# Kernel optimization log

Measured on AMD Instinct MI355X. Metric: run time of the kernel, lower is better.

The kernel has to match this reference:

```python
import jax, jax.numpy as jnp
import numpy as np

HEAD_NUM = 7
HEAD_DIM = 64
HIDDEN = 896

def rotate_half(t):
    d = t.shape[-1] // 2
    return jnp.concatenate([-t[..., d:], t[..., :d]], axis=-1)

def setup_inputs() -> dict:
    key = jax.random.key(0)
    ks = jax.random.split(key, 11)
    B, S = 4, 2048
    proj = HEAD_NUM * HEAD_DIM  # 448
    sc_in = 1.0 / np.sqrt(HIDDEN)
    sc_pr = 1.0 / np.sqrt(proj)
    pos = jnp.arange(S)[:, None].astype(jnp.float32)
    inv_freq = 1.0 / (10000.0 ** (jnp.arange(0, HEAD_DIM, 2, dtype=jnp.float32) / HEAD_DIM))
    ang = pos * inv_freq[None, :]              # [S, D/2]
    emb = jnp.concatenate([ang, ang], axis=-1) # [S, D]
    return {
        'x': jax.random.normal(ks[0], (B, S, HIDDEN), jnp.float32),
        'cos': jnp.cos(emb),
        'sin': jnp.sin(emb),
        'q_w': jax.random.normal(ks[1], (proj, HIDDEN), jnp.float32) * sc_in,
        'q_b': jax.random.normal(ks[2], (proj,), jnp.float32) * 0.01,
        'k_w': jax.random.normal(ks[3], (proj, HIDDEN), jnp.float32) * sc_in,
        'k_b': jax.random.normal(ks[4], (proj,), jnp.float32) * 0.01,
        'v_w': jax.random.normal(ks[5], (proj, HIDDEN), jnp.float32) * sc_in,
        'v_b': jax.random.normal(ks[6], (proj,), jnp.float32) * 0.01,
        'o_w': jax.random.normal(ks[7], (HIDDEN, proj), jnp.float32) * sc_pr,
        'o_b': jax.random.normal(ks[8], (HIDDEN,), jnp.float32) * 0.01,
    }

def reference(x, cos, sin, q_w, q_b, k_w, k_b, v_w, v_b, o_w, o_b):
    B, S, _ = x.shape
    def proj(w, b):
        y = jnp.einsum('bsh,ph->bsp', x, w) + b          # [B,S,H*D]
        return y.reshape(B, S, HEAD_NUM, HEAD_DIM).transpose(0, 2, 1, 3)  # [B,H,S,D]
    q = proj(q_w, q_b)
    k = proj(k_w, k_b)
    v = proj(v_w, v_b)
    c = cos[None, None, :, :]
    s = sin[None, None, :, :]
    q = q * c + rotate_half(q) * s
    k = k * c + rotate_half(k) * s
    scores = jnp.einsum('bhqd,bhkd->bhqk', q, k) / np.sqrt(HEAD_DIM)
    attn = jax.nn.softmax(scores, axis=-1)
    out = jnp.einsum('bhqk,bhkd->bhqd', attn, v)          # [B,H,S,D]
    out = out.transpose(0, 2, 1, 3).reshape(B, S, HEAD_NUM * HEAD_DIM)
    return jnp.einsum('bsp,hp->bsh', out, o_w) + o_b
```

## Files before the change

kernel.cpp:

```cpp
#include <hip/hip_runtime.h>

typedef _Float16 f16;
typedef __attribute__((ext_vector_type(8))) _Float16 f16x8;
typedef __attribute__((ext_vector_type(4))) _Float16 f16x4;
typedef __attribute__((ext_vector_type(4))) float f32x4;

#define MFMA(a,b,c) __builtin_amdgcn_mfma_f32_16x16x32_f16(a,b,c,0,0,0)

constexpr int HN = 7, HD = 64, HID = 896, PR = 448;
constexpr int NB = 4, NS = 2048, NM = NB * NS;
constexpr float LOG2E = 1.44269504088896f;

__device__ __forceinline__ void gload16(const f16* g, f16* l) {
    __builtin_amdgcn_global_load_lds(
        (const __attribute__((address_space(1))) void*)g,
        (__attribute__((address_space(3))) void*)l,
        16, 0, 0);
}

__global__ __launch_bounds__(256) void conv_kernel(
    const float* __restrict__ x,  const float* __restrict__ qw,
    const float* __restrict__ kw, const float* __restrict__ vw,
    const float* __restrict__ ow,
    f16* __restrict__ xb, f16* __restrict__ wq, f16* __restrict__ wk,
    f16* __restrict__ wv, f16* __restrict__ wo)
{
    const int XV = NM * HID / 4;
    const int WV = PR * HID / 4;
    const int TOT = XV + 4 * WV;
    int64_t stride = (int64_t)gridDim.x * blockDim.x;
    for (int64_t v = (int64_t)blockIdx.x * 256 + threadIdx.x; v < TOT; v += stride) {
        const float* src; f16* dst; int64_t off;
        if (v < XV)               { src = x;  dst = xb; off = v; }
        else if (v < XV + WV)     { src = qw; dst = wq; off = v - XV; }
        else if (v < XV + 2*WV)   { src = kw; dst = wk; off = v - XV - WV; }
        else if (v < XV + 3*WV)   { src = vw; dst = wv; off = v - XV - 2*WV; }
        else                      { src = ow; dst = wo; off = v - XV - 3*WV; }
        f32x4 fv = *((const f32x4*)src + off);
        f16x4 hv = { (f16)fv[0], (f16)fv[1], (f16)fv[2], (f16)fv[3] };
        *((f16x4*)dst + off) = hv;
    }
}

__global__ __launch_bounds__(256) void qkv_gemm(
    const f16* __restrict__ xb, const f16* __restrict__ wq,
    const f16* __restrict__ wk, const f16* __restrict__ wv,
    const float* __restrict__ qb, const float* __restrict__ kb,
    const float* __restrict__ vb,
    const float* __restrict__ cosT, const float* __restrict__ sinT,
    f16* __restrict__ Q, f16* __restrict__ K, f16* __restrict__ Vt)
{
    extern __shared__ char smem[];
    f16*  As = (f16*)smem;
    f16*  Bs = (f16*)(smem + 128*64*2);
    float* Cs = (float*)smem;

    const int ty = blockIdx.x / 7;
    const int nt = blockIdx.x % 7;
    const int mt = blockIdx.y;
    const int m0 = mt * 128, n0 = nt * 64;

    const f16* w = (ty == 0) ? wq : (ty == 1) ? wk : wv;
    const float* bias = (ty == 0) ? qb : (ty == 1) ? kb : vb;

    const int tid = threadIdx.x;
    const int wid = tid >> 6, lane = tid & 63;
    const int wm = wid >> 1, wn = wid & 1;
    const int lg = lane >> 4, lr = lane & 15;

    f32x4 acc[4][2] = {};

    for (int k0 = 0; k0 < HID; k0 += 64) {
        #pragma unroll
        for (int p = 0; p < 4; p++) {
            int r = p*32 + (tid >> 3), c = tid & 7;
            f16x8 v = *(const f16x8*)(xb + (int64_t)(m0 + r)*HID + k0 + c*8);
            *(f16x8*)(As + r*64 + ((c ^ (r & 7)) * 8)) = v;
        }
        #pragma unroll
        for (int p = 0; p < 2; p++) {
            int r = p*32 + (tid >> 3), c = tid & 7;
            f16x8 v = *(const f16x8*)(w + (int64_t)(n0 + r)*HID + k0 + c*8);
            *(f16x8*)(Bs + r*64 + ((c ^ (r & 7)) * 8)) = v;
        }
        __syncthreads();
        #pragma unroll
        for (int kc = 0; kc < 2; kc++) {
            f16x8 af[4], bf[2];
            #pragma unroll
            for (int fm = 0; fm < 4; fm++) {
                int r = wm*64 + fm*16 + lr;
                int c = kc*4 + lg;
                af[fm] = *(const f16x8*)(As + r*64 + ((c ^ (r & 7)) * 8));
            }
            #pragma unroll
            for (int fn = 0; fn < 2; fn++) {
                int r = wn*32 + fn*16 + lr;
                int c = kc*4 + lg;
                bf[fn] = *(const f16x8*)(Bs + r*64 + ((c ^ (r & 7)) * 8));
            }
            #pragma unroll
            for (int fm = 0; fm < 4; fm++)
                #pragma unroll
                for (int fn = 0; fn < 2; fn++)
                    acc[fm][fn] = MFMA(af[fm], bf[fn], acc[fm][fn]);
        }
        __syncthreads();
    }

    #pragma unroll
    for (int fm = 0; fm < 4; fm++)
        #pragma unroll
        for (int fn = 0; fn < 2; fn++)
            #pragma unroll
            for (int j = 0; j < 4; j++) {
                int r = wm*64 + fm*16 + lg*4 + j;
                int c = wn*32 + fn*16 + lr;
                Cs[r*65 + c] = acc[fm][fn][j] + bias[n0 + c];
            }
    __syncthreads();

    const int b = m0 / NS;
    const int s0 = m0 % NS;
    const int64_t bhbase = ((int64_t)(b*HN + nt)) * NS * HD;
    if (ty < 2) {
        const float scale = (ty == 0) ? 0.125f * LOG2E : 1.0f;
        int r = tid >> 1, d0 = (tid & 1) * 32;
        int s = s0 + r;
        f16 vals[32];
        #pragma unroll
        for (int i = 0; i < 32; i++) {
            int d = d0 + i;
            float y  = Cs[r*65 + d];
            float yo = Cs[r*65 + (d ^ 32)];
            float rot = (d < 32) ? -yo : yo;
            float val = (y * cosT[s*64 + d] + rot * sinT[s*64 + d]) * scale;
            vals[i] = (f16)val;
        }
        if (ty == 0) {
            f16* p = Q + bhbase + (int64_t)s * HD + d0;
            #pragma unroll
            for (int i = 0; i < 4; i++)
                *(f16x8*)(p + i*8) = *(f16x8*)(vals + i*8);
        } else {
            int tt = (s0 >> 6) + (r >> 6);
            int rt = r & 63;
            f16* base = K + bhbase + tt*4096 + rt*64;
            #pragma unroll
            for (int i = 0; i < 4; i++) {
                int pos = ((d0 >> 3) + i) ^ (rt & 7);
                *(f16x8*)(base + pos*8) = *(f16x8*)(vals + i*8);
            }
        }
    } else {
        int d = tid >> 2, si = (tid & 3) * 32;
        f16 vals[32];
        #pragma unroll
        for (int i = 0; i < 32; i++)
            vals[i] = (f16)Cs[(si + i)*65 + d];
        int tt = (s0 >> 6) + (si >> 6);
        int sb = si & 63;
        f16* base = Vt + bhbase + tt*4096 + d*64;
        #pragma unroll
        for (int i = 0; i < 4; i++) {
            int pos = ((sb >> 3) + i) ^ (d & 7);
            *(f16x8*)(base + pos*8) = *(f16x8*)(vals + i*8);
        }
    }
}

__global__ __launch_bounds__(256) void attn_kernel(
    const f16* __restrict__ Q, const f16* __restrict__ K2,
    const f16* __restrict__ V2, f16* __restrict__ O)
{
    __shared__ __align__(16) f16 KVs[2][2][4096];
    __shared__ __align__(16) f16 Pl[4][16][72];

    const int qb = blockIdx.x, bh = blockIdx.y;
    const int tid = threadIdx.x, w = tid >> 6, lane = tid & 63;
    const int g = lane >> 4, lr = lane & 15;
    const int q0 = qb * 64 + w * 16;

    const int64_t bhoff = (int64_t)bh * NS * HD;
    const f16* Qp = Q + bhoff;
    const f16* Kp = K2 + bhoff;
    const f16* Vp = V2 + bhoff;

    f16x8 aq0 = *(const f16x8*)(Qp + (q0 + lr) * HD + g * 8);
    f16x8 aq1 = *(const f16x8*)(Qp + (q0 + lr) * HD + 32 + g * 8);

    const int stoff = w * 1024 + lane * 8;
    const int ldoff = w * 1024;

    gload16(Kp + stoff,       &KVs[0][0][ldoff]);
    gload16(Kp + stoff + 512, &KVs[0][0][ldoff + 512]);
    gload16(Vp + stoff,       &KVs[0][1][ldoff]);
    gload16(Vp + stoff + 512, &KVs[0][1][ldoff + 512]);
    __syncthreads();

    f32x4 accO[4] = {};
    float mrun = -1e30f, srun = 0.f;

    const int ch0 = (g ^ (lr & 7)) * 8;
    const int ch1 = ((4 + g) ^ (lr & 7)) * 8;

    int buf = 0;
    for (int t = 0; t < NS / 64; ++t) {
        if (t + 1 < NS / 64) {
            const f16* ks = Kp + (t + 1) * 4096 + stoff;
            const f16* vs = Vp + (t + 1) * 4096 + stoff;
            gload16(ks,       &KVs[buf ^ 1][0][ldoff]);
            gload16(ks + 512, &KVs[buf ^ 1][0][ldoff + 512]);
            gload16(vs,       &KVs[buf ^ 1][1][ldoff]);
            gload16(vs + 512, &KVs[buf ^ 1][1][ldoff + 512]);
        }
        const f16* Ks = &KVs[buf][0][0];
        const f16* Vs = &KVs[buf][1][0];

        f32x4 sf[4];
        #pragma unroll
        for (int kt = 0; kt < 4; ++kt) {
            const f16* kl = Ks + (kt * 16 + lr) * 64;
            f16x8 k0 = *(const f16x8*)(kl + ch0);
            f16x8 k1 = *(const f16x8*)(kl + ch1);
            f32x4 z = {};
            z = MFMA(k0, aq0, z);
            z = MFMA(k1, aq1, z);
            sf[kt] = z;
        }

        float m00 = fmaxf(fmaxf(sf[0][0], sf[0][1]), fmaxf(sf[0][2], sf[0][3]));
        float m01 = fmaxf(fmaxf(sf[1][0], sf[1][1]), fmaxf(sf[1][2], sf[1][3]));
        float m10 = fmaxf(fmaxf(sf[2][0], sf[2][1]), fmaxf(sf[2][2], sf[2][3]));
        float m11 = fmaxf(fmaxf(sf[3][0], sf[3][1]), fmaxf(sf[3][2], sf[3][3]));
        float pmax = fmaxf(fmaxf(m00, m01), fmaxf(m10, m11));
        pmax = fmaxf(pmax, __shfl_xor(pmax, 16, 64));
        pmax = fmaxf(pmax, __shfl_xor(pmax, 32, 64));

        float mn = fmaxf(mrun, pmax);
        float corr = exp2f(mrun - mn);
        mrun = mn;

        float pf[16];
        #pragma unroll
        for (int kt = 0; kt < 4; ++kt)
            #pragma unroll
            for (int j = 0; j < 4; ++j)
                pf[kt*4 + j] = exp2f(sf[kt][j] - mn);

        float s0a = (pf[0] + pf[1]) + (pf[2] + pf[3]);
        float s1a = (pf[4] + pf[5]) + (pf[6] + pf[7]);
        float s2a = (pf[8] + pf[9]) + (pf[10] + pf[11]);
        float s3a = (pf[12] + pf[13]) + (pf[14] + pf[15]);
        float tsum = (s0a + s1a) + (s2a + s3a);
        tsum += __shfl_xor(tsum, 16, 64);
        tsum += __shfl_xor(tsum, 32, 64);
        srun = srun * corr + tsum;

        #pragma unroll
        for (int fn = 0; fn < 4; ++fn)
            #pragma unroll
            for (int j = 0; j < 4; ++j)
                accO[fn][j] *= corr;

        #pragma unroll
        for (int kt = 0; kt < 4; ++kt) {
            f16x4 pk = { (f16)pf[kt*4+0], (f16)pf[kt*4+1], (f16)pf[kt*4+2], (f16)pf[kt*4+3] };
            *(f16x4*)&Pl[w][lr][kt*16 + g*4] = pk;
        }
        f16x8 p0 = *(const f16x8*)&Pl[w][lr][g * 8];
        f16x8 p1 = *(const f16x8*)&Pl[w][lr][32 + g * 8];

        #pragma unroll
        for (int fn = 0; fn < 4; ++fn) {
            const f16* vl = Vs + (fn * 16 + lr) * 64;
            f16x8 v0 = *(const f16x8*)(vl + ch0);
            f16x8 v1 = *(const f16x8*)(vl + ch1);
            accO[fn] = MFMA(v0, p0, accO[fn]);
            accO[fn] = MFMA(v1, p1, accO[fn]);
        }
        __syncthreads();
        buf ^= 1;
    }

    const int b = bh / HN, h = bh % HN;
    const float inv = 1.0f / srun;
    const int q = q0 + lr;
    f16* orow = O + ((int64_t)b * NS + q) * PR + h * HD;
    #pragma unroll
    for (int fn = 0; fn < 4; ++fn) {
        f16x4 hv = { (f16)(accO[fn][0] * inv), (f16)(accO[fn][1] * inv),
                     (f16)(accO[fn][2] * inv), (f16)(accO[fn][3] * inv) };
        *(f16x4*)(orow + fn * 16 + g * 4) = hv;
    }
}

__global__ __launch_bounds__(256) void oproj_gemm(
    const f16* __restrict__ Ob, const f16* __restrict__ wo,
    const float* __restrict__ ob, float* __restrict__ out)
{
    extern __shared__ char smem[];
    f16* As = (f16*)smem;
    f16* Bs = (f16*)(smem + 128*64*2);

    const int nt = blockIdx.x, mt = blockIdx.y;
    const int m0 = mt*128, n0 = nt*64;
    const int tid = threadIdx.x;
    const int wid = tid >> 6, lane = tid & 63;
    const int wm = wid >> 1, wn = wid & 1;
    const int lg = lane >> 4, lr = lane & 15;

    f32x4 acc[4][2] = {};

    for (int k0 = 0; k0 < PR; k0 += 64) {
        #pragma unroll
        for (int p = 0; p < 4; p++) {
            int r = p*32 + (tid >> 3), c = tid & 7;
            f16x8 v = *(const f16x8*)(Ob + (int64_t)(m0 + r)*PR + k0 + c*8);
            *(f16x8*)(As + r*64 + ((c ^ (r & 7)) * 8)) = v;
        }
        #pragma unroll
        for (int p = 0; p < 2; p++) {
            int r = p*32 + (tid >> 3), c = tid & 7;
            f16x8 v = *(const f16x8*)(wo + (int64_t)(n0 + r)*PR + k0 + c*8);
            *(f16x8*)(Bs + r*64 + ((c ^ (r & 7)) * 8)) = v;
        }
        __syncthreads();
        #pragma unroll
        for (int kc = 0; kc < 2; kc++) {
            f16x8 af[4], bf[2];
            #pragma unroll
            for (int fm = 0; fm < 4; fm++) {
                int r = wm*64 + fm*16 + lr;
                int c = kc*4 + lg;
                af[fm] = *(const f16x8*)(As + r*64 + ((c ^ (r & 7)) * 8));
            }
            #pragma unroll
            for (int fn = 0; fn < 2; fn++) {
                int r = wn*32 + fn*16 + lr;
                int c = kc*4 + lg;
                bf[fn] = *(const f16x8*)(Bs + r*64 + ((c ^ (r & 7)) * 8));
            }
            #pragma unroll
            for (int fm = 0; fm < 4; fm++)
                #pragma unroll
                for (int fn = 0; fn < 2; fn++)
                    acc[fm][fn] = MFMA(af[fm], bf[fn], acc[fm][fn]);
        }
        __syncthreads();
    }

    #pragma unroll
    for (int fm = 0; fm < 4; fm++)
        #pragma unroll
        for (int fn = 0; fn < 2; fn++)
            #pragma unroll
            for (int j = 0; j < 4; j++) {
                int row = m0 + wm*64 + fm*16 + lg*4 + j;
                int col = n0 + wn*32 + fn*16 + lr;
                out[(int64_t)row*HID + col] = acc[fm][fn][j] + ob[col];
            }
}

extern "C" void kernel_launch(void* const* d_in, const int* in_sizes, int n_in,
                              void* d_out, int out_size, void* d_ws, size_t ws_size,
                              hipStream_t stream) {
    const float* x    = (const float*)d_in[0];
    const float* cosT = (const float*)d_in[1];
    const float* sinT = (const float*)d_in[2];
    const float* qw   = (const float*)d_in[3];
    const float* qb   = (const float*)d_in[4];
    const float* kw   = (const float*)d_in[5];
    const float* kb   = (const float*)d_in[6];
    const float* vw   = (const float*)d_in[7];
    const float* vb   = (const float*)d_in[8];
    const float* ow   = (const float*)d_in[9];
    const float* ob   = (const float*)d_in[10];
    float* out = (float*)d_out;

    char* ws = (char*)d_ws;
    f16* xb = (f16*)ws;  ws += (size_t)NM * HID * 2;
    f16* wqf = (f16*)ws; ws += (size_t)PR * HID * 2;
    f16* wkf = (f16*)ws; ws += (size_t)PR * HID * 2;
    f16* wvf = (f16*)ws; ws += (size_t)PR * HID * 2;
    f16* wof = (f16*)ws; ws += (size_t)HID * PR * 2;
    f16* Qb = (f16*)ws;  ws += (size_t)NB * HN * NS * HD * 2;
    f16* Kb = (f16*)ws;  ws += (size_t)NB * HN * NS * HD * 2;
    f16* Vt = (f16*)ws;  ws += (size_t)NB * HN * HD * NS * 2;
    f16* Obuf = (f16*)ws; ws += (size_t)NM * PR * 2;

    conv_kernel<<<dim3(2048), dim3(256), 0, stream>>>(x, qw, kw, vw, ow, xb, wqf, wkf, wvf, wof);
    qkv_gemm<<<dim3(21, 64), dim3(256), 33280, stream>>>(xb, wqf, wkf, wvf, qb, kb, vb, cosT, sinT, Qb, Kb, Vt);
    attn_kernel<<<dim3(32, 28), dim3(256), 0, stream>>>(Qb, Kb, Vt, Obuf);
    oproj_gemm<<<dim3(14, 64), dim3(256), 24576, stream>>>(Obuf, wof, ob, out);
}
```

Baseline: 256.6 us.

## Enlarge GEMM tiles, use direct LDS loads, XCD swizzle, lazy softmax rescale

The QKV and output-projection GEMMs get larger tiles (256x64 and 128x128) with 4x4 MFMA fragments per wave, and load global memory straight into LDS. The QKV epilogue now stages results in fp16 and handles full rows with vectorized cos/sin reads. All three main kernels remap block indices so neighbouring tiles land on the same XCD, which should improve L2 reuse. The attention kernel raises wave priority around its MFMA sections and skips the running-max rescale unless the max grows by more than a threshold. Staging in fp16 and the lazy rescale trade some numerical headroom for less work, and the larger tiles cut the number of blocks, which can leave CUs underused.

Result: no change. 254.5 us (-0.8%).

```diff
diff --git a/kernel.cpp b/kernel.cpp
--- a/kernel.cpp
+++ b/kernel.cpp
@@ -16,6 +16,10 @@
         (const __attribute__((address_space(1))) void*)g,
         (__attribute__((address_space(3))) void*)l,
         16, 0, 0);
+}
+
+__device__ __forceinline__ int xcd_swz(int orig, int per) {
+    return (orig & 7) * per + (orig >> 3);
 }
 
 __global__ __launch_bounds__(256) void conv_kernel(
@@ -51,121 +55,125 @@
     f16* __restrict__ Q, f16* __restrict__ K, f16* __restrict__ Vt)
 {
     extern __shared__ char smem[];
-    f16*  As = (f16*)smem;
-    f16*  Bs = (f16*)(smem + 128*64*2);
-    float* Cs = (float*)smem;
-
-    const int ty = blockIdx.x / 7;
-    const int nt = blockIdx.x % 7;
-    const int mt = blockIdx.y;
-    const int m0 = mt * 128, n0 = nt * 64;
+    f16* As = (f16*)smem;
+    f16* Bs = (f16*)(smem + 256*64*2);
+    f16* Cs = (f16*)smem;
+
+    const int wg = xcd_swz(blockIdx.x, 84);
+    const int tynt = wg % 21, mt = wg / 21;
+    const int ty = tynt / 7, nt = tynt % 7;
+    const int m0 = mt * 256, n0 = nt * 64;
 
     const f16* w = (ty == 0) ? wq : (ty == 1) ? wk : wv;
     const float* bias = (ty == 0) ? qb : (ty == 1) ? kb : vb;
 
     const int tid = threadIdx.x;
-    const int wid = tid >> 6, lane = tid & 63;
-    const int wm = wid >> 1, wn = wid & 1;
-    const int lg = lane >> 4, lr = lane & 15;
-
-    f32x4 acc[4][2] = {};
+    const int wv_ = tid >> 6, lane = tid & 63;
+    const int g = lane >> 4, lr = lane & 15;
+    const int lrow = lane >> 3;
+    const int cswz = (lane & 7) ^ (lrow & 7);
+
+    const int ch0 = ((0*4 + g) ^ (lr & 7)) * 8;
+    const int ch1 = ((1*4 + g) ^ (lr & 7)) * 8;
+
+    f32x4 acc[4][4] = {};
 
     for (int k0 = 0; k0 < HID; k0 += 64) {
         #pragma unroll
-        for (int p = 0; p < 4; p++) {
-            int r = p*32 + (tid >> 3), c = tid & 7;
-            f16x8 v = *(const f16x8*)(xb + (int64_t)(m0 + r)*HID + k0 + c*8);
-            *(f16x8*)(As + r*64 + ((c ^ (r & 7)) * 8)) = v;
+        for (int p = 0; p < 8; p++) {
+            int rt = wv_*64 + p*8;
+            gload16(xb + (int64_t)(m0 + rt + lrow)*HID + k0 + cswz*8, As + rt*64);
         }
         #pragma unroll
         for (int p = 0; p < 2; p++) {
-            int r = p*32 + (tid >> 3), c = tid & 7;
-            f16x8 v = *(const f16x8*)(w + (int64_t)(n0 + r)*HID + k0 + c*8);
-            *(f16x8*)(Bs + r*64 + ((c ^ (r & 7)) * 8)) = v;
+            int rt = wv_*16 + p*8;
+            gload16(w + (int64_t)(n0 + rt + lrow)*HID + k0 + cswz*8, Bs + rt*64);
         }
         __syncthreads();
         #pragma unroll
         for (int kc = 0; kc < 2; kc++) {
-            f16x8 af[4], bf[2];
-            #pragma unroll
-            for (int fm = 0; fm < 4; fm++) {
-                int r = wm*64 + fm*16 + lr;
-                int c = kc*4 + lg;
-                af[fm] = *(const f16x8*)(As + r*64 + ((c ^ (r & 7)) * 8));
-            }
-            #pragma unroll
-            for (int fn = 0; fn < 2; fn++) {
-                int r = wn*32 + fn*16 + lr;
-                int c = kc*4 + lg;
-                bf[fn] = *(const f16x8*)(Bs + r*64 + ((c ^ (r & 7)) * 8));
-            }
+            const int ch = kc ? ch1 : ch0;
+            f16x8 af[4], bf[4];
+            #pragma unroll
+            for (int fm = 0; fm < 4; fm++)
+                af[fm] = *(const f16x8*)(As + (wv_*64 + fm*16 + lr)*64 + ch);
+            #pragma unroll
+            for (int fn = 0; fn < 4; fn++)
+                bf[fn] = *(const f16x8*)(Bs + (fn*16 + lr)*64 + ch);
             #pragma unroll
             for (int fm = 0; fm < 4; fm++)
                 #pragma unroll
-                for (int fn = 0; fn < 2; fn++)
+                for (int fn = 0; fn < 4; fn++)
                     acc[fm][fn] = MFMA(af[fm], bf[fn], acc[fm][fn]);
         }
         __syncthreads();
     }
 
+    float bias_f[4];
+    #pragma unroll
+    for (int fn = 0; fn < 4; fn++) bias_f[fn] = bias[n0 + fn*16 + lr];
     #pragma unroll
     for (int fm = 0; fm < 4; fm++)
         #pragma unroll
-        for (int fn = 0; fn < 2; fn++)
-            #pragma unroll
-            for (int j = 0; j < 4; j++) {
-                int r = wm*64 + fm*16 + lg*4 + j;
-                int c = wn*32 + fn*16 + lr;
-                Cs[r*65 + c] = acc[fm][fn][j] + bias[n0 + c];
-            }
+        for (int fn = 0; fn < 4; fn++)
+            #pragma unroll
+            for (int j = 0; j < 4; j++)
+                Cs[(wv_*64 + fm*16 + g*4 + j)*72 + fn*16 + lr] = (f16)(acc[fm][fn][j] + bias_f[fn]);
     __syncthreads();
 
     const int b = m0 / NS;
     const int s0 = m0 % NS;
     const int64_t bhbase = ((int64_t)(b*HN + nt)) * NS * HD;
+
     if (ty < 2) {
         const float scale = (ty == 0) ? 0.125f * LOG2E : 1.0f;
-        int r = tid >> 1, d0 = (tid & 1) * 32;
-        int s = s0 + r;
-        f16 vals[32];
-        #pragma unroll
-        for (int i = 0; i < 32; i++) {
-            int d = d0 + i;
-            float y  = Cs[r*65 + d];
-            float yo = Cs[r*65 + (d ^ 32)];
-            float rot = (d < 32) ? -yo : yo;
-            float val = (y * cosT[s*64 + d] + rot * sinT[s*64 + d]) * scale;
-            vals[i] = (f16)val;
+        const int r = tid, s = s0 + r;
+        const f16* crow = Cs + r*72;
+        const float* cr = cosT + s*64;
+        const float* sr = sinT + s*64;
+        f16 vals[64];
+        #pragma unroll
+        for (int i = 0; i < 4; i++) {
+            f16x8 ylo = *(const f16x8*)(crow + i*8);
+            f16x8 yhi = *(const f16x8*)(crow + 32 + i*8);
+            #pragma unroll
+            for (int h = 0; h < 2; h++) {
+                f32x4 cl = *(const f32x4*)(cr + i*8 + h*4);
+                f32x4 sl = *(const f32x4*)(sr + i*8 + h*4);
+                f32x4 chh = *(const f32x4*)(cr + 32 + i*8 + h*4);
+                f32x4 shh = *(const f32x4*)(sr + 32 + i*8 + h*4);
+                #pragma unroll
+                for (int j = 0; j < 4; j++) {
+                    float lo = (float)ylo[h*4+j], hi = (float)yhi[h*4+j];
+                    vals[i*8 + h*4 + j]      = (f16)((lo*cl[j] - hi*sl[j]) * scale);
+                    vals[32 + i*8 + h*4 + j] = (f16)((hi*chh[j] + lo*shh[j]) * scale);
+                }
+            }
         }
         if (ty == 0) {
-            f16* p = Q + bhbase + (int64_t)s * HD + d0;
-            #pragma unroll
-            for (int i = 0; i < 4; i++)
+            f16* p = Q + bhbase + (int64_t)s * HD;
+            #pragma unroll
+            for (int i = 0; i < 8; i++)
                 *(f16x8*)(p + i*8) = *(f16x8*)(vals + i*8);
         } else {
             int tt = (s0 >> 6) + (r >> 6);
             int rt = r & 63;
             f16* base = K + bhbase + tt*4096 + rt*64;
             #pragma unroll
-            for (int i = 0; i < 4; i++) {
-                int pos = ((d0 >> 3) + i) ^ (rt & 7);
-                *(f16x8*)(base + pos*8) = *(f16x8*)(vals + i*8);
-            }
+            for (int i = 0; i < 8; i++)
+                *(f16x8*)(base + (i ^ (rt & 7))*8) = *(f16x8*)(vals + i*8);
         }
     } else {
-        int d = tid >> 2, si = (tid & 3) * 32;
-        f16 vals[32];
-        #pragma unroll
-        for (int i = 0; i < 32; i++)
-            vals[i] = (f16)Cs[(si + i)*65 + d];
-        int tt = (s0 >> 6) + (si >> 6);
-        int sb = si & 63;
+        const int d = tid & 63, sblk = tid >> 6, si0 = sblk * 64;
+        f16 vals[64];
+        #pragma unroll
+        for (int i = 0; i < 64; i++)
+            vals[i] = Cs[(si0 + i)*72 + d];
+        int tt = (s0 >> 6) + sblk;
         f16* base = Vt + bhbase + tt*4096 + d*64;
         #pragma unroll
-        for (int i = 0; i < 4; i++) {
-            int pos = ((sb >> 3) + i) ^ (d & 7);
-            *(f16x8*)(base + pos*8) = *(f16x8*)(vals + i*8);
-        }
+        for (int i = 0; i < 8; i++)
+            *(f16x8*)(base + (i ^ (d & 7))*8) = *(f16x8*)(vals + i*8);
     }
 }
 
@@ -176,7 +184,8 @@
     __shared__ __align__(16) f16 KVs[2][2][4096];
     __shared__ __align__(16) f16 Pl[4][16][72];
 
-    const int qb = blockIdx.x, bh = blockIdx.y;
+    const int wg = xcd_swz(blockIdx.x, 112);
+    const int qb = wg % 32, bh = wg / 32;
     const int tid = threadIdx.x, w = tid >> 6, lane = tid & 63;
     const int g = lane >> 4, lr = lane & 15;
     const int q0 = qb * 64 + w * 16;
@@ -218,6 +227,7 @@
         const f16* Vs = &KVs[buf][1][0];
 
         f32x4 sf[4];
+        __builtin_amdgcn_s_setprio(1);
         #pragma unroll
         for (int kt = 0; kt < 4; ++kt) {
             const f16* kl = Ks + (kt * 16 + lr) * 64;
@@ -228,25 +238,34 @@
             z = MFMA(k1, aq1, z);
             sf[kt] = z;
         }
-
-        float m00 = fmaxf(fmaxf(sf[0][0], sf[0][1]), fmaxf(sf[0][2], sf[0][3]));
-        float m01 = fmaxf(fmaxf(sf[1][0], sf[1][1]), fmaxf(sf[1][2], sf[1][3]));
-        float m10 = fmaxf(fmaxf(sf[2][0], sf[2][1]), fmaxf(sf[2][2], sf[2][3]));
-        float m11 = fmaxf(fmaxf(sf[3][0], sf[3][1]), fmaxf(sf[3][2], sf[3][3]));
-        float pmax = fmaxf(fmaxf(m00, m01), fmaxf(m10, m11));
+        __builtin_amdgcn_s_setprio(0);
+
+        float m0a = fmaxf(fmaxf(sf[0][0], sf[0][1]), fmaxf(sf[0][2], sf[0][3]));
+        float m1a = fmaxf(fmaxf(sf[1][0], sf[1][1]), fmaxf(sf[1][2], sf[1][3]));
+        float m2a = fmaxf(fmaxf(sf[2][0], sf[2][1]), fmaxf(sf[2][2], sf[2][3]));
+        float m3a = fmaxf(fmaxf(sf[3][0], sf[3][1]), fmaxf(sf[3][2], sf[3][3]));
+        float pmax = fmaxf(fmaxf(m0a, m1a), fmaxf(m2a, m3a));
         pmax = fmaxf(pmax, __shfl_xor(pmax, 16, 64));
         pmax = fmaxf(pmax, __shfl_xor(pmax, 32, 64));
 
-        float mn = fmaxf(mrun, pmax);
-        float corr = exp2f(mrun - mn);
-        mrun = mn;
+        if (!__all(pmax - mrun <= 8.0f)) {
+            float mn = fmaxf(mrun, pmax);
+            float corr = exp2f(mrun - mn);
+            mrun = mn;
+            srun *= corr;
+            #pragma unroll
+            for (int fn = 0; fn < 4; ++fn)
+                #pragma unroll
+                for (int j = 0; j < 4; ++j)
+                    accO[fn][j] *= corr;
+        }
 
         float pf[16];
         #pragma unroll
         for (int kt = 0; kt < 4; ++kt)
             #pragma unroll
             for (int j = 0; j < 4; ++j)
-                pf[kt*4 + j] = exp2f(sf[kt][j] - mn);
+                pf[kt*4 + j] = exp2f(sf[kt][j] - mrun);
 
         float s0a = (pf[0] + pf[1]) + (pf[2] + pf[3]);
         float s1a = (pf[4] + pf[5]) + (pf[6] + pf[7]);
@@ -255,13 +274,7 @@
         float tsum = (s0a + s1a) + (s2a + s3a);
         tsum += __shfl_xor(tsum, 16, 64);
         tsum += __shfl_xor(tsum, 32, 64);
-        srun = srun * corr + tsum;
-
-        #pragma unroll
-        for (int fn = 0; fn < 4; ++fn)
-            #pragma unroll
-            for (int j = 0; j < 4; ++j)
-                accO[fn][j] *= corr;
+        srun += tsum;
 
         #pragma unroll
         for (int kt = 0; kt < 4; ++kt) {
@@ -271,6 +284,7 @@
         f16x8 p0 = *(const f16x8*)&Pl[w][lr][g * 8];
         f16x8 p1 = *(const f16x8*)&Pl[w][lr][32 + g * 8];
 
+        __builtin_amdgcn_s_setprio(1);
         #pragma unroll
         for (int fn = 0; fn < 4; ++fn) {
             const f16* vl = Vs + (fn * 16 + lr) * 64;
@@ -279,6 +293,7 @@
             accO[fn] = MFMA(v0, p0, accO[fn]);
             accO[fn] = MFMA(v1, p1, accO[fn]);
         }
+        __builtin_amdgcn_s_setprio(0);
         __syncthreads();
         buf ^= 1;
     }
@@ -303,62 +318,64 @@
     f16* As = (f16*)smem;
     f16* Bs = (f16*)(smem + 128*64*2);
 
-    const int nt = blockIdx.x, mt = blockIdx.y;
-    const int m0 = mt*128, n0 = nt*64;
+    const int wg = xcd_swz(blockIdx.x, 56);
+    const int nt = wg % 7, mt = wg / 7;
+    const int m0 = mt*128, n0 = nt*128;
     const int tid = threadIdx.x;
-    const int wid = tid >> 6, lane = tid & 63;
-    const int wm = wid >> 1, wn = wid & 1;
-    const int lg = lane >> 4, lr = lane & 15;
-
-    f32x4 acc[4][2] = {};
+    const int wv_ = tid >> 6, lane = tid & 63;
+    const int wm = wv_ >> 1, wn = wv_ & 1;
+    const int g = lane >> 4, lr = lane & 15;
+    const int lrow = lane >> 3;
+    const int cswz = (lane & 7) ^ (lrow & 7);
+
+    const int ch0 = (g ^ (lr & 7)) * 8;
+    const int ch1 = ((4 + g) ^ (lr & 7)) * 8;
+
+    f32x4 acc[4][4] = {};
 
     for (int k0 = 0; k0 < PR; k0 += 64) {
         #pragma unroll
         for (int p = 0; p < 4; p++) {
-            int r = p*32 + (tid >> 3), c = tid & 7;
-            f16x8 v = *(const f16x8*)(Ob + (int64_t)(m0 + r)*PR + k0 + c*8);
-            *(f16x8*)(As + r*64 + ((c ^ (r & 7)) * 8)) = v;
-        }
-        #pragma unroll
-        for (int p = 0; p < 2; p++) {
-            int r = p*32 + (tid >> 3), c = tid & 7;
-            f16x8 v = *(const f16x8*)(wo + (int64_t)(n0 + r)*PR + k0 + c*8);
-            *(f16x8*)(Bs + r*64 + ((c ^ (r & 7)) * 8)) = v;
+            int rt = wv_*32 + p*8;
+            gload16(Ob + (int64_t)(m0 + rt + lrow)*PR + k0 + cswz*8, As + rt*64);
+        }
+        #pragma unroll
+        for (int p = 0; p < 4; p++) {
+            int rt = wv_*32 + p*8;
+            gload16(wo + (int64_t)(n0 + rt + lrow)*PR + k0 + cswz*8, Bs + rt*64);
         }
         __syncthreads();
         #pragma unroll
         for (int kc = 0; kc < 2; kc++) {
-            f16x8 af[4], bf[2];
-            #pragma unroll
-            for (int fm = 0; fm < 4; fm++) {
-                int r = wm*64 + fm*16 + lr;
-                int c = kc*4 + lg;
-                af[fm] = *(const f16x8*)(As + r*64 + ((c ^ (r & 7)) * 8));
-            }
-            #pragma unroll
-            for (int fn = 0; fn < 2; fn++) {
-                int r = wn*32 + fn*16 + lr;
-                int c = kc*4 + lg;
-                bf[fn] = *(const f16x8*)(Bs + r*64 + ((c ^ (r & 7)) * 8));
-            }
+            const int ch = kc ? ch1 : ch0;
+            f16x8 af[4], bf[4];
+            #pragma unroll
+            for (int fm = 0; fm < 4; fm++)
+                af[fm] = *(const f16x8*)(As + (wm*64 + fm*16 + lr)*64 + ch);
+            #pragma unroll
+            for (int fn = 0; fn < 4; fn++)
+                bf[fn] = *(const f16x8*)(Bs + (wn*64 + fn*16 + lr)*64 + ch);
             #pragma unroll
             for (int fm = 0; fm < 4; fm++)
                 #pragma unroll
-                for (int fn = 0; fn < 2; fn++)
+                for (int fn = 0; fn < 4; fn++)
                     acc[fm][fn] = MFMA(af[fm], bf[fn], acc[fm][fn]);
         }
         __syncthreads();
     }
 
+    float bias_f[4];
+    #pragma unroll
+    for (int fn = 0; fn < 4; fn++) bias_f[fn] = ob[n0 + wn*64 + fn*16 + lr];
     #pragma unroll
     for (int fm = 0; fm < 4; fm++)
         #pragma unroll
-        for (int fn = 0; fn < 2; fn++)
+        for (int fn = 0; fn < 4; fn++)
             #pragma unroll
             for (int j = 0; j < 4; j++) {
-                int row = m0 + wm*64 + fm*16 + lg*4 + j;
-                int col = n0 + wn*32 + fn*16 + lr;
-                out[(int64_t)row*HID + col] = acc[fm][fn][j] + ob[col];
+                int row = m0 + wm*64 + fm*16 + g*4 + j;
+                int col = n0 + wn*64 + fn*16 + lr;
+                out[(int64_t)row*HID + col] = acc[fm][fn][j] + bias_f[fn];
             }
 }
 
@@ -390,7 +407,7 @@
     f16* Obuf = (f16*)ws; ws += (size_t)NM * PR * 2;
 
     conv_kernel<<<dim3(2048), dim3(256), 0, stream>>>(x, qw, kw, vw, ow, xb, wqf, wkf, wvf, wof);
-    qkv_gemm<<<dim3(21, 64), dim3(256), 33280, stream>>>(xb, wqf, wkf, wvf, qb, kb, vb, cosT, sinT, Qb, Kb, Vt);
-    attn_kernel<<<dim3(32, 28), dim3(256), 0, stream>>>(Qb, Kb, Vt, Obuf);
-    oproj_gemm<<<dim3(14, 64), dim3(256), 24576, stream>>>(Obuf, wof, ob, out);
-}
+    qkv_gemm<<<dim3(672), dim3(256), 40960, stream>>>(xb, wqf, wkf, wvf, qb, kb, vb, cosT, sinT, Qb, Kb, Vt);
+    attn_kernel<<<dim3(896), dim3(256), 0, stream>>>(Qb, Kb, Vt, Obuf);
+    oproj_gemm<<<dim3(448), dim3(256), 32768, stream>>>(Obuf, wof, ob, out);
+}
```
